# Performance work log

Hardware: AMD Instinct MI355X
Metric: run time of the kernel (lower is better)

The kernel has to match this reference:

```python
import jax, jax.numpy as jnp
import numpy as np
import math

D_MODEL = 1024
NUM_HEADS = 16
D_K = D_MODEL // NUM_HEADS


def setup_inputs() -> dict:
    key = jax.random.key(0)
    ks = jax.random.split(key, 9)
    s = 1.0 / math.sqrt(D_MODEL)
    x = jax.random.normal(ks[0], (2, 2048, D_MODEL), dtype=jnp.float32)
    # torch Linear params: weight [out, in], bias [out]
    Wq = jax.random.uniform(ks[1], (D_MODEL, D_MODEL), jnp.float32, -s, s)
    bq = jax.random.uniform(ks[2], (D_MODEL,), jnp.float32, -s, s)
    Wk = jax.random.uniform(ks[3], (D_MODEL, D_MODEL), jnp.float32, -s, s)
    bk = jax.random.uniform(ks[4], (D_MODEL,), jnp.float32, -s, s)
    Wv = jax.random.uniform(ks[5], (D_MODEL, D_MODEL), jnp.float32, -s, s)
    bv = jax.random.uniform(ks[6], (D_MODEL,), jnp.float32, -s, s)
    Wo = jax.random.uniform(ks[7], (D_MODEL, D_MODEL), jnp.float32, -s, s)
    bo = jax.random.uniform(ks[8], (D_MODEL,), jnp.float32, -s, s)
    return {"x": x, "Wq": Wq, "bq": bq, "Wk": Wk, "bk": bk,
            "Wv": Wv, "bv": bv, "Wo": Wo, "bo": bo}


def reference(x, Wq, bq, Wk, bk, Wv, bv, Wo, bo):
    B, T, _ = x.shape
    scale = 1.0 / math.sqrt(D_MODEL)  # NOTE: module scales by sqrt(d_model), not sqrt(d_k)

    def proj(W, b):
        # torch Linear: x @ W^T + b, then split heads -> [B, H, T, d_k]
        y = jnp.einsum('btd,ed->bte', x, W) + b
        return y.reshape(B, T, NUM_HEADS, D_K).transpose(0, 2, 1, 3)

    Q = proj(Wq, bq)
    K = proj(Wk, bk)
    V = proj(Wv, bv)
    logits = jnp.einsum('bhtd,bhsd->bhts', Q, K) * scale  # [B,H,T,T]
    attn = jax.nn.softmax(logits, axis=-1)
    out = jnp.einsum('bhts,bhsd->bhtd', attn, V)  # [B,H,T,d_k]
    out = out.transpose(0, 2, 1, 3).reshape(B, T, D_MODEL)
    return jnp.einsum('btd,ed->bte', out, Wo) + bo
```

## Files before the change

kernel.cpp:

```cpp
#include <hip/hip_runtime.h>

#define T_SEQ 2048
#define NB 2
#define NH 16
#define DK 64
#define DMODEL 1024

typedef __bf16 bf16x8 __attribute__((ext_vector_type(8)));
typedef float f32x4 __attribute__((ext_vector_type(4)));
typedef unsigned short ushortx8 __attribute__((ext_vector_type(8)));
typedef unsigned short ushortx4 __attribute__((ext_vector_type(4)));

__device__ inline unsigned short f2b1(float f) {
  unsigned u = __float_as_uint(f);
  u += 0x7fffu + ((u >> 16) & 1u);
  return (unsigned short)(u >> 16);
}

__device__ inline void gload16(const void* g, void* l) {
  __builtin_amdgcn_global_load_lds((const __attribute__((address_space(1))) void*)g,
                                   (__attribute__((address_space(3))) void*)l, 16, 0, 0);
}

__device__ inline bf16x8 mk8(unsigned a, unsigned b, unsigned c, unsigned d) {
  uint4 t = {a, b, c, d};
  return *(bf16x8*)&t;
}

__device__ inline unsigned cvtpk(float lo, float hi) {
  unsigned r;
  asm("v_cvt_pk_bf16_f32 %0, %1, %2" : "=v"(r) : "v"(lo), "v"(hi));
  return r;
}

__global__ void prep(const float* __restrict__ x,
                     const float* __restrict__ w0, const float* __restrict__ w1,
                     const float* __restrict__ w2, const float* __restrict__ w3,
                     const float* __restrict__ bq, const float* __restrict__ bk,
                     const float* __restrict__ bv,
                     unsigned short* __restrict__ xb, unsigned short* __restrict__ Wqkv,
                     float* __restrict__ bqkv) {
  int bid = blockIdx.x, tid = threadIdx.x;
  if (bid < 4096) {
    int i = (bid * 256 + tid) * 4;
    float4 v = *(const float4*)(x + i);
    ushortx4 o;
    o.x = f2b1(v.x); o.y = f2b1(v.y); o.z = f2b1(v.z); o.w = f2b1(v.w);
    *(ushortx4*)(xb + i) = o;
  } else if (bid < 8192) {
    int which = (bid - 4096) >> 10;
    int i = (((bid - 4096) & 1023) * 256 + tid) * 4;
    const float* src = which == 0 ? w0 : which == 1 ? w1 : which == 2 ? w2 : w3;
    float4 v = *(const float4*)(src + i);
    ushortx4 o;
    o.x = f2b1(v.x); o.y = f2b1(v.y); o.z = f2b1(v.z); o.w = f2b1(v.w);
    *(ushortx4*)(Wqkv + (long)which * 1048576 + i) = o;
  } else {
    int i = (bid - 8192) * 256 + tid;
    if (i < 3072) {
      float v = (i < 1024) ? bq[i] : (i < 2048 ? bk[i - 1024] : bv[i - 2048]);
      bqkv[i] = v;
    }
  }
}

__global__ __launch_bounds__(256, 3)
void gemm_qkv(const unsigned short* __restrict__ A, const unsigned short* __restrict__ B,
              const float* __restrict__ bias, unsigned short* __restrict__ Cb,
              unsigned short* __restrict__ Vt, int M, int N, int K, float scl) {
  __shared__ unsigned short As[2][4096];
  __shared__ unsigned short Bs[2][4096];
  const int tid = threadIdx.x;
  const int w = tid >> 6, lane = tid & 63;
  const int quad = lane >> 4, l16 = lane & 15;
  const int bm = blockIdx.y, bn = blockIdx.x;
  const int wm = w >> 1, wn = w & 1;

  f32x4 acc[4][4] = {};

  const int srow = tid >> 2;
  const int c4 = tid & 3;
  const unsigned short* aG = A + (long)(bm * 128 + srow) * K + c4 * 8;
  const unsigned short* bG = B + (long)(bn * 128 + srow) * K + c4 * 8;
  const long rs64 = (long)64 * K;
  const int wo = w * 512;

  gload16(aG, As[0] + wo);
  gload16(aG + rs64, As[0] + 2048 + wo);
  gload16(bG, Bs[0] + wo);
  gload16(bG + rs64, Bs[0] + 2048 + wo);

  int buf = 0;
  for (int kt = 0; kt < K; kt += 32) {
    __syncthreads();
    {
      const int nb = buf ^ 1;
      gload16(aG + kt + 32, As[nb] + wo);
      gload16(aG + rs64 + kt + 32, As[nb] + 2048 + wo);
      gload16(bG + kt + 32, Bs[nb] + wo);
      gload16(bG + rs64 + kt + 32, Bs[nb] + 2048 + wo);
    }

    bf16x8 af[4], bfr[4];
#pragma unroll
    for (int mt = 0; mt < 4; mt++)
      af[mt] = *(const bf16x8*)(As[buf] + (wm * 64 + mt * 16 + l16) * 32 + quad * 8);
#pragma unroll
    for (int nt = 0; nt < 4; nt++)
      bfr[nt] = *(const bf16x8*)(Bs[buf] + (wn * 64 + nt * 16 + l16) * 32 + quad * 8);
#pragma unroll
    for (int mt = 0; mt < 4; mt++)
#pragma unroll
      for (int nt = 0; nt < 4; nt++)
        acc[mt][nt] = __builtin_amdgcn_mfma_f32_16x16x32_bf16(af[mt], bfr[nt], acc[mt][nt], 0, 0, 0);
    buf ^= 1;
  }

  const int col0 = bn * 128 + wn * 64 + l16;
  const bool isV = (bn * 128) >= 2048;
#pragma unroll
  for (int mt = 0; mt < 4; mt++) {
    int row0 = bm * 128 + wm * 64 + mt * 16 + quad * 4;
#pragma unroll
    for (int nt = 0; nt < 4; nt++) {
      int col = col0 + nt * 16;
      float bb = bias[col];
      float s = (col < 1024) ? scl : 1.0f;
      if (!isV) {
#pragma unroll
        for (int r = 0; r < 4; r++)
          Cb[(long)(row0 + r) * N + col] = f2b1((acc[mt][nt][r] + bb) * s);
      } else {
        int cv = col - 2048;
        int h = cv >> 6, d = cv & 63;
        int b = row0 >> 11, t0 = row0 & 2047;
        ushortx4 o;
        o.x = f2b1(acc[mt][nt][0] + bb);
        o.y = f2b1(acc[mt][nt][1] + bb);
        o.z = f2b1(acc[mt][nt][2] + bb);
        o.w = f2b1(acc[mt][nt][3] + bb);
        *(ushortx4*)(Vt + ((long)((b * NH + h) * DK + d)) * T_SEQ + t0) = o;
      }
    }
  }
}

__global__ __launch_bounds__(256, 2)
void gemm_out(const unsigned short* __restrict__ A, const unsigned short* __restrict__ B,
              const float* __restrict__ bias, float* __restrict__ Cf, int M, int N, int K) {
  __shared__ unsigned short As[2][2048];
  __shared__ unsigned short Bs[2][4096];
  const int tid = threadIdx.x;
  const int w = tid >> 6, lane = tid & 63;
  const int quad = lane >> 4, l16 = lane & 15;
  const int bm = blockIdx.y, bn = blockIdx.x;
  const int wm = w >> 1, wn = w & 1;

  f32x4 acc[2][4] = {};

  const int srow = tid >> 2;
  const int c4 = tid & 3;
  const unsigned short* aG = A + (long)(bm * 64 + srow) * K + c4 * 8;
  const unsigned short* bG = B + (long)(bn * 128 + srow) * K + c4 * 8;
  const long rs64 = (long)64 * K;
  const int wo = w * 512;

  gload16(aG, As[0] + wo);
  gload16(bG, Bs[0] + wo);
  gload16(bG + rs64, Bs[0] + 2048 + wo);

  int buf = 0;
  for (int kt = 0; kt < K; kt += 32) {
    __syncthreads();
    {
      const int nb = buf ^ 1;
      gload16(aG + kt + 32, As[nb] + wo);
      gload16(bG + kt + 32, Bs[nb] + wo);
      gload16(bG + rs64 + kt + 32, Bs[nb] + 2048 + wo);
    }

    bf16x8 af[2], bfr[4];
#pragma unroll
    for (int mt = 0; mt < 2; mt++)
      af[mt] = *(const bf16x8*)(As[buf] + (wm * 32 + mt * 16 + l16) * 32 + quad * 8);
#pragma unroll
    for (int nt = 0; nt < 4; nt++)
      bfr[nt] = *(const bf16x8*)(Bs[buf] + (wn * 64 + nt * 16 + l16) * 32 + quad * 8);
#pragma unroll
    for (int mt = 0; mt < 2; mt++)
#pragma unroll
      for (int nt = 0; nt < 4; nt++)
        acc[mt][nt] = __builtin_amdgcn_mfma_f32_16x16x32_bf16(af[mt], bfr[nt], acc[mt][nt], 0, 0, 0);
    buf ^= 1;
  }

  const int col0 = bn * 128 + wn * 64 + l16;
#pragma unroll
  for (int mt = 0; mt < 2; mt++) {
    int row0 = bm * 64 + wm * 32 + mt * 16 + quad * 4;
#pragma unroll
    for (int nt = 0; nt < 4; nt++) {
      int col = col0 + nt * 16;
      float bb = bias[col];
#pragma unroll
      for (int r = 0; r < 4; r++)
        Cf[(long)(row0 + r) * N + col] = acc[mt][nt][r] + bb;
    }
  }
}

__global__ __launch_bounds__(256, 4)
void attn3(const unsigned short* __restrict__ QKV, const unsigned short* __restrict__ Vt,
           unsigned short* __restrict__ Onum, float* __restrict__ Oden) {
  __shared__ unsigned short Ks[2][4096];
  __shared__ unsigned short Vs[2][4096];
  const int tid = threadIdx.x;
  const int w = tid >> 6, lane = tid & 63;
  const int quad = lane >> 4, l16 = lane & 15;

  const int id = blockIdx.x;
  const int group = (id & 7) | (((id >> 3) & 7) << 3);
  const int qt = id >> 6;
  const int bh = group >> 1, split = group & 1;
  const int b = bh >> 4, h = bh & 15;
  const long qkvBase = (long)b * T_SEQ * 3072;
  const int kv0 = split * 1024;

  bf16x8 qf[2][2];
#pragma unroll
  for (int g = 0; g < 2; g++) {
    const unsigned short* qp = QKV + qkvBase + (long)(qt * 128 + w * 32 + g * 16 + l16) * 3072 + h * 64 + quad * 8;
    qf[g][0] = *(const bf16x8*)qp;
    qf[g][1] = *(const bf16x8*)(qp + 32);
  }

  const unsigned short* kG[2];
  const unsigned short* vG[2];
#pragma unroll
  for (int i = 0; i < 2; i++) {
    int S = w * 128 + i * 64 + lane;
    int row = S >> 3;
    int c = (S & 7) ^ (row & 7);
    kG[i] = QKV + qkvBase + 1024 + h * 64 + (long)(kv0 + row) * 3072 + c * 8;
    vG[i] = Vt + (long)bh * DK * T_SEQ + (long)row * T_SEQ + kv0 + c * 8;
  }
  const int wo2 = w * 1024;

  gload16(kG[0], Ks[0] + wo2);
  gload16(kG[1], Ks[0] + wo2 + 512);
  gload16(vG[0], Vs[0] + wo2);
  gload16(vG[1], Vs[0] + wo2 + 512);
  kG[0] += 64 * 3072; kG[1] += 64 * 3072;
  vG[0] += 64;        vG[1] += 64;

  const unsigned onesu = 0x3F803F80u;
  const bf16x8 ones = mk8(onesu, onesu, onesu, onesu);

  f32x4 acco[2][4] = {};
  f32x4 accp[2] = {};
  int buf = 0;
  const int e16 = (l16 & 7) * 16;

  for (int it = 0; it < 16; it++) {
    __syncthreads();
    {
      const int nb = buf ^ 1;
      gload16(kG[0], Ks[nb] + wo2);
      gload16(kG[1], Ks[nb] + wo2 + 512);
      gload16(vG[0], Vs[nb] + wo2);
      gload16(vG[1], Vs[nb] + wo2 + 512);
      kG[0] += 64 * 3072; kG[1] += 64 * 3072;
      vG[0] += 64;        vG[1] += 64;
    }

    f32x4 st[2][4];
    __builtin_amdgcn_s_setprio(1);
#pragma unroll
    for (int nt = 0; nt < 4; nt++) {
      const char* kr = (char*)(Ks[buf]) + (nt * 16 + l16) * 128;
      bf16x8 k0 = *(const bf16x8*)(kr + ((quad * 16) ^ e16));
      bf16x8 k1 = *(const bf16x8*)(kr + (((quad + 4) * 16) ^ e16));
#pragma unroll
      for (int g = 0; g < 2; g++) {
        f32x4 z = {};
        z = __builtin_amdgcn_mfma_f32_16x16x32_bf16(k0, qf[g][0], z, 0, 0, 0);
        z = __builtin_amdgcn_mfma_f32_16x16x32_bf16(k1, qf[g][1], z, 0, 0, 0);
        st[g][nt] = z;
      }
    }
    __builtin_amdgcn_s_setprio(0);

    bf16x8 pa[2][2];
#pragma unroll
    for (int g = 0; g < 2; g++) {
      unsigned pk[4][2];
#pragma unroll
      for (int nt = 0; nt < 4; nt++) {
        float p0 = __builtin_amdgcn_exp2f(st[g][nt][0]);
        float p1 = __builtin_amdgcn_exp2f(st[g][nt][1]);
        float p2 = __builtin_amdgcn_exp2f(st[g][nt][2]);
        float p3 = __builtin_amdgcn_exp2f(st[g][nt][3]);
        pk[nt][0] = cvtpk(p0, p1);
        pk[nt][1] = cvtpk(p2, p3);
      }
      pa[g][0] = mk8(pk[0][0], pk[0][1], pk[1][0], pk[1][1]);
      pa[g][1] = mk8(pk[2][0], pk[2][1], pk[3][0], pk[3][1]);
      accp[g] = __builtin_amdgcn_mfma_f32_16x16x32_bf16(pa[g][0], ones, accp[g], 0, 0, 0);
      accp[g] = __builtin_amdgcn_mfma_f32_16x16x32_bf16(pa[g][1], ones, accp[g], 0, 0, 0);
    }

    const int off8 = (quad & 1) * 8;
    const int cq = quad >> 1;
    __builtin_amdgcn_s_setprio(1);
#pragma unroll
    for (int nt = 0; nt < 4; nt++) {
      const char* vr = (char*)(Vs[buf]) + (nt * 16 + l16) * 128;
#pragma unroll
      for (int km = 0; km < 2; km++) {
        uint2 lo = *(const uint2*)(vr + (((km * 4 + cq) * 16) ^ e16) + off8);
        uint2 hi = *(const uint2*)(vr + (((km * 4 + cq + 2) * 16) ^ e16) + off8);
        bf16x8 vf = mk8(lo.x, lo.y, hi.x, hi.y);
#pragma unroll
        for (int g = 0; g < 2; g++)
          acco[g][nt] = __builtin_amdgcn_mfma_f32_16x16x32_bf16(pa[g][km], vf, acco[g][nt], 0, 0, 0);
      }
    }
    __builtin_amdgcn_s_setprio(0);
    buf ^= 1;
  }

  const long rowBase = (long)bh * T_SEQ + qt * 128 + w * 32;
  const long numBase = ((long)split * 65536 + rowBase) * 64;
  if (l16 == 0) {
    *(f32x4*)(Oden + (long)split * 65536 + rowBase + quad * 4) = accp[0];
    *(f32x4*)(Oden + (long)split * 65536 + rowBase + 16 + quad * 4) = accp[1];
  }
#pragma unroll
  for (int g = 0; g < 2; g++) {
#pragma unroll
    for (int nt = 0; nt < 4; nt++)
#pragma unroll
      for (int r = 0; r < 4; r++)
        Onum[numBase + (long)(g * 16 + quad * 4 + r) * 64 + nt * 16 + l16] = f2b1(acco[g][nt][r]);
  }
}

__global__ __launch_bounds__(256)
void combine(const unsigned short* __restrict__ Onum, const float* __restrict__ Oden,
             unsigned short* __restrict__ Ob) {
  int idx = blockIdx.x * 256 + threadIdx.x;
  int rp = idx >> 4;
  int dq = (idx & 15) * 4;
  ushortx4 n0 = *(const ushortx4*)(Onum + (long)rp * 64 + dq);
  ushortx4 n1 = *(const ushortx4*)(Onum + 4194304L + (long)rp * 64 + dq);
  float den = Oden[rp] + Oden[65536 + rp];
  float rl = __builtin_amdgcn_rcpf(den);
  int bh = rp >> 11, t = rp & 2047;
  int b = bh >> 4, h = bh & 15;
  ushortx4 o;
  o.x = f2b1((__uint_as_float((unsigned)n0.x << 16) + __uint_as_float((unsigned)n1.x << 16)) * rl);
  o.y = f2b1((__uint_as_float((unsigned)n0.y << 16) + __uint_as_float((unsigned)n1.y << 16)) * rl);
  o.z = f2b1((__uint_as_float((unsigned)n0.z << 16) + __uint_as_float((unsigned)n1.z << 16)) * rl);
  o.w = f2b1((__uint_as_float((unsigned)n0.w << 16) + __uint_as_float((unsigned)n1.w << 16)) * rl);
  *(ushortx4*)(Ob + (long)(b * T_SEQ + t) * DMODEL + h * 64 + dq) = o;
}

extern "C" void kernel_launch(void* const* d_in, const int* in_sizes, int n_in,
                              void* d_out, int out_size, void* d_ws, size_t ws_size,
                              hipStream_t stream) {
  const float* x  = (const float*)d_in[0];
  const float* Wq = (const float*)d_in[1];
  const float* bq = (const float*)d_in[2];
  const float* Wk = (const float*)d_in[3];
  const float* bk = (const float*)d_in[4];
  const float* Wv = (const float*)d_in[5];
  const float* bv = (const float*)d_in[6];
  const float* Wo = (const float*)d_in[7];
  const float* bo = (const float*)d_in[8];
  float* out = (float*)d_out;

  unsigned short* xb   = (unsigned short*)d_ws;
  unsigned short* Wqkv = xb + 4194304;
  unsigned short* Wob  = Wqkv + 3145728;
  float*          bqkv = (float*)(Wob + 1048576);
  unsigned short* QKV  = (unsigned short*)(bqkv + 3072);
  unsigned short* Vt   = QKV + 12582912;
  unsigned short* Ob   = Vt + 4194304;
  unsigned short* Onum = Ob + 4194304;
  float*          Oden = (float*)(Onum + 8388608);

  prep<<<8204, 256, 0, stream>>>(x, Wq, Wk, Wv, Wo, bq, bk, bv, xb, Wqkv, bqkv);

  gemm_qkv<<<dim3(24, 32), 256, 0, stream>>>(xb, Wqkv, bqkv, QKV, Vt,
                                             4096, 3072, 1024, 0.04508422037f);

  attn3<<<dim3(1024), 256, 0, stream>>>(QKV, Vt, Onum, Oden);
  combine<<<dim3(4096), 256, 0, stream>>>(Onum, Oden, Ob);

  gemm_out<<<dim3(8, 64), 256, 0, stream>>>(Ob, Wob, bo, out, 4096, 1024, 1024);
}
```

Measured before the change: 192.2 us.

## Drop KV split in attention, fuse normalization and remove combine kernel

The attention kernel now processes the full 2048-key range per block instead of splitting it in two, then normalizes the output in-register and writes the final bf16 result directly. This removes the separate combine kernel and the round trip of partial numerators and denominators through global memory. The V-transpose layout written by the QKV GEMM is permuted along t so the attention kernel can read V fragments with a single 16-byte LDS load instead of two 8-byte loads. In exchange the grid halves to 512 blocks with twice the loop length and a lower occupancy hint, which may reduce parallelism and latency hiding.

```diff
diff --git a/kernel.cpp b/kernel.cpp
--- a/kernel.cpp
+++ b/kernel.cpp
@@ -134,12 +134,14 @@
         int cv = col - 2048;
         int h = cv >> 6, d = cv & 63;
         int b = row0 >> 11, t0 = row0 & 2047;
+        int a = (t0 & 31) >> 2;
+        int t0p = (t0 & ~31) | ((a & 3) << 3) | ((a >> 2) << 2);
         ushortx4 o;
         o.x = f2b1(acc[mt][nt][0] + bb);
         o.y = f2b1(acc[mt][nt][1] + bb);
         o.z = f2b1(acc[mt][nt][2] + bb);
         o.w = f2b1(acc[mt][nt][3] + bb);
-        *(ushortx4*)(Vt + ((long)((b * NH + h) * DK + d)) * T_SEQ + t0) = o;
+        *(ushortx4*)(Vt + ((long)((b * NH + h) * DK + d)) * T_SEQ + t0p) = o;
       }
     }
   }
@@ -209,9 +211,9 @@
   }
 }
 
-__global__ __launch_bounds__(256, 4)
+__global__ __launch_bounds__(256, 2)
 void attn3(const unsigned short* __restrict__ QKV, const unsigned short* __restrict__ Vt,
-           unsigned short* __restrict__ Onum, float* __restrict__ Oden) {
+           unsigned short* __restrict__ Ob) {
   __shared__ unsigned short Ks[2][4096];
   __shared__ unsigned short Vs[2][4096];
   const int tid = threadIdx.x;
@@ -219,12 +221,10 @@
   const int quad = lane >> 4, l16 = lane & 15;
 
   const int id = blockIdx.x;
-  const int group = (id & 7) | (((id >> 3) & 7) << 3);
-  const int qt = id >> 6;
-  const int bh = group >> 1, split = group & 1;
+  const int bh = id & 31;
+  const int qt = id >> 5;
   const int b = bh >> 4, h = bh & 15;
   const long qkvBase = (long)b * T_SEQ * 3072;
-  const int kv0 = split * 1024;
 
   bf16x8 qf[2][2];
 #pragma unroll
@@ -241,8 +241,8 @@
     int S = w * 128 + i * 64 + lane;
     int row = S >> 3;
     int c = (S & 7) ^ (row & 7);
-    kG[i] = QKV + qkvBase + 1024 + h * 64 + (long)(kv0 + row) * 3072 + c * 8;
-    vG[i] = Vt + (long)bh * DK * T_SEQ + (long)row * T_SEQ + kv0 + c * 8;
+    kG[i] = QKV + qkvBase + 1024 + h * 64 + (long)row * 3072 + c * 8;
+    vG[i] = Vt + (long)bh * DK * T_SEQ + (long)row * T_SEQ + c * 8;
   }
   const int wo2 = w * 1024;
 
@@ -261,9 +261,9 @@
   int buf = 0;
   const int e16 = (l16 & 7) * 16;
 
-  for (int it = 0; it < 16; it++) {
+  for (int it = 0; it < 32; it++) {
     __syncthreads();
-    {
+    if (it < 31) {
       const int nb = buf ^ 1;
       gload16(kG[0], Ks[nb] + wo2);
       gload16(kG[1], Ks[nb] + wo2 + 512);
@@ -309,17 +309,13 @@
       accp[g] = __builtin_amdgcn_mfma_f32_16x16x32_bf16(pa[g][1], ones, accp[g], 0, 0, 0);
     }
 
-    const int off8 = (quad & 1) * 8;
-    const int cq = quad >> 1;
     __builtin_amdgcn_s_setprio(1);
 #pragma unroll
     for (int nt = 0; nt < 4; nt++) {
       const char* vr = (char*)(Vs[buf]) + (nt * 16 + l16) * 128;
 #pragma unroll
       for (int km = 0; km < 2; km++) {
-        uint2 lo = *(const uint2*)(vr + (((km * 4 + cq) * 16) ^ e16) + off8);
-        uint2 hi = *(const uint2*)(vr + (((km * 4 + cq + 2) * 16) ^ e16) + off8);
-        bf16x8 vf = mk8(lo.x, lo.y, hi.x, hi.y);
+        bf16x8 vf = *(const bf16x8*)(vr + (((km * 4 + quad) * 16) ^ e16));
 #pragma unroll
         for (int g = 0; g < 2; g++)
           acco[g][nt] = __builtin_amdgcn_mfma_f32_16x16x32_bf16(pa[g][km], vf, acco[g][nt], 0, 0, 0);
@@ -329,40 +325,20 @@
     buf ^= 1;
   }
 
-  const long rowBase = (long)bh * T_SEQ + qt * 128 + w * 32;
-  const long numBase = ((long)split * 65536 + rowBase) * 64;
-  if (l16 == 0) {
-    *(f32x4*)(Oden + (long)split * 65536 + rowBase + quad * 4) = accp[0];
-    *(f32x4*)(Oden + (long)split * 65536 + rowBase + 16 + quad * 4) = accp[1];
-  }
+  const int t0 = qt * 128 + w * 32;
 #pragma unroll
   for (int g = 0; g < 2; g++) {
+    f32x4 rl;
+#pragma unroll
+    for (int r = 0; r < 4; r++) rl[r] = __builtin_amdgcn_rcpf(accp[g][r]);
 #pragma unroll
     for (int nt = 0; nt < 4; nt++)
 #pragma unroll
-      for (int r = 0; r < 4; r++)
-        Onum[numBase + (long)(g * 16 + quad * 4 + r) * 64 + nt * 16 + l16] = f2b1(acco[g][nt][r]);
-  }
-}
-
-__global__ __launch_bounds__(256)
-void combine(const unsigned short* __restrict__ Onum, const float* __restrict__ Oden,
-             unsigned short* __restrict__ Ob) {
-  int idx = blockIdx.x * 256 + threadIdx.x;
-  int rp = idx >> 4;
-  int dq = (idx & 15) * 4;
-  ushortx4 n0 = *(const ushortx4*)(Onum + (long)rp * 64 + dq);
-  ushortx4 n1 = *(const ushortx4*)(Onum + 4194304L + (long)rp * 64 + dq);
-  float den = Oden[rp] + Oden[65536 + rp];
-  float rl = __builtin_amdgcn_rcpf(den);
-  int bh = rp >> 11, t = rp & 2047;
-  int b = bh >> 4, h = bh & 15;
-  ushortx4 o;
-  o.x = f2b1((__uint_as_float((unsigned)n0.x << 16) + __uint_as_float((unsigned)n1.x << 16)) * rl);
-  o.y = f2b1((__uint_as_float((unsigned)n0.y << 16) + __uint_as_float((unsigned)n1.y << 16)) * rl);
-  o.z = f2b1((__uint_as_float((unsigned)n0.z << 16) + __uint_as_float((unsigned)n1.z << 16)) * rl);
-  o.w = f2b1((__uint_as_float((unsigned)n0.w << 16) + __uint_as_float((unsigned)n1.w << 16)) * rl);
-  *(ushortx4*)(Ob + (long)(b * T_SEQ + t) * DMODEL + h * 64 + dq) = o;
+      for (int r = 0; r < 4; r++) {
+        int t = t0 + g * 16 + quad * 4 + r;
+        Ob[(long)(b * T_SEQ + t) * DMODEL + h * 64 + nt * 16 + l16] = f2b1(acco[g][nt][r] * rl[r]);
+      }
+  }
 }
 
 extern "C" void kernel_launch(void* const* d_in, const int* in_sizes, int n_in,
@@ -386,16 +362,13 @@
   unsigned short* QKV  = (unsigned short*)(bqkv + 3072);
   unsigned short* Vt   = QKV + 12582912;
   unsigned short* Ob   = Vt + 4194304;
-  unsigned short* Onum = Ob + 4194304;
-  float*          Oden = (float*)(Onum + 8388608);
 
   prep<<<8204, 256, 0, stream>>>(x, Wq, Wk, Wv, Wo, bq, bk, bv, xb, Wqkv, bqkv);
 
   gemm_qkv<<<dim3(24, 32), 256, 0, stream>>>(xb, Wqkv, bqkv, QKV, Vt,
                                              4096, 3072, 1024, 0.04508422037f);
 
-  attn3<<<dim3(1024), 256, 0, stream>>>(QKV, Vt, Onum, Oden);
-  combine<<<dim3(4096), 256, 0, stream>>>(Onum, Oden, Ob);
+  attn3<<<dim3(512), 256, 0, stream>>>(QKV, Vt, Ob);
 
   gemm_out<<<dim3(8, 64), 256, 0, stream>>>(Ob, Wob, bo, out, 4096, 1024, 1024);
 }
```

After: 186.0 us. 3.2% less time.
